# Kernel optimization log

Hardware: AMD Instinct MI355X
Metric: run time of the kernel (lower is better)

## Reference

```python
import jax, jax.numpy as jnp
import numpy as np

N_NODES = 100000
N_EDGES = 1600000
EMB = 128
N_LAYER = 5
X_DIM = 178
E_DIM = 18
BN_EPS = 1e-5


def setup_inputs() -> dict:
    key = jax.random.key(0)
    ks = jax.random.split(key, 20)
    s = 0.05  # weight scale
    inp = {}
    inp["x"] = jax.random.normal(ks[0], (N_NODES, X_DIM), jnp.float32)
    inp["edge_attr"] = jax.random.uniform(ks[1], (N_EDGES, E_DIM), jnp.float32)
    # input MLP (178 -> emb -> emb, LeakyReLU 0.1)
    inp["iw1"] = jax.random.normal(ks[2], (X_DIM, EMB), jnp.float32) * s
    inp["ib1"] = jax.random.normal(ks[3], (EMB,), jnp.float32) * s
    inp["iw2"] = jax.random.normal(ks[4], (EMB, EMB), jnp.float32) * s
    inp["ib2"] = jax.random.normal(ks[5], (EMB,), jnp.float32) * s
    # per-layer edge embedding MLP (18 -> emb -> emb, LeakyReLU 0.1)
    inp["ew1"] = jax.random.normal(ks[6], (N_LAYER, E_DIM, EMB), jnp.float32) * s
    inp["eb1"] = jax.random.normal(ks[7], (N_LAYER, EMB), jnp.float32) * s
    inp["ew2"] = jax.random.normal(ks[8], (N_LAYER, EMB, EMB), jnp.float32) * s
    inp["eb2"] = jax.random.normal(ks[9], (N_LAYER, EMB), jnp.float32) * s
    # per-layer GIN update MLP (emb -> 2emb -> emb, ReLU)
    inp["mw1"] = jax.random.normal(ks[10], (N_LAYER, EMB, 2 * EMB), jnp.float32) * s
    inp["mb1"] = jax.random.normal(ks[11], (N_LAYER, 2 * EMB), jnp.float32) * s
    inp["mw2"] = jax.random.normal(ks[12], (N_LAYER, 2 * EMB, EMB), jnp.float32) * s
    inp["mb2"] = jax.random.normal(ks[13], (N_LAYER, EMB), jnp.float32) * s
    # per-layer BatchNorm affine params
    inp["gamma"] = jnp.ones((N_LAYER, EMB), jnp.float32)
    inp["beta"] = jnp.zeros((N_LAYER, EMB), jnp.float32)
    inp["edge_index"] = jax.random.randint(ks[14], (2, N_EDGES), 0, N_NODES)
    return inp


def _leaky(v):
    return jnp.where(v > 0, v, 0.1 * v)


def reference(x, edge_attr, iw1, ib1, iw2, ib2, ew1, eb1, ew2, eb2,
              mw1, mb1, mw2, mb2, gamma, beta, edge_index):
    src = edge_index[0]  # x_j gathered from source nodes (PyG source_to_target)
    dst = edge_index[1]
    n = x.shape[0]

    # input node MLP with LeakyReLU(0.1)
    h = _leaky(x @ iw1 + ib1) @ iw2 + ib2  # [N, EMB]

    for l in range(N_LAYER):
        # edge embeddings for real edges: [E, EMB]
        ee = _leaky(edge_attr @ ew1[l] + eb1[l]) @ ew2[l] + eb2[l]
        # self-loop edges have zero edge_attr -> constant embedding vector [EMB]
        self_e = _leaky(eb1[l]) @ ew2[l] + eb2[l]
        # message = x_j + edge_emb; aggregate (add) at destination, plus self-loop term
        msg = h[src] + ee
        aggr = jax.ops.segment_sum(msg, dst, num_segments=n) + h + self_e
        # GIN update MLP (ReLU)
        hh = jnp.maximum(aggr @ mw1[l] + mb1[l], 0.0) @ mw2[l] + mb2[l]
        # BatchNorm1d (training mode: batch stats, biased variance)
        mean = hh.mean(axis=0)
        var = hh.var(axis=0)
        hh = (hh - mean) / jnp.sqrt(var + BN_EPS) * gamma[l] + beta[l]
        if l < N_LAYER - 1:
            hh = jnp.maximum(hh, 0.0)  # ReLU on all but last layer; dropout p=0 is a no-op
        h = hh

    return h  # JK == 'last'
```

## Files before the change

### kernel.cpp

```cpp
#include <hip/hip_runtime.h>
#include <hip/hip_bf16.h>
#include <hip/hip_fp16.h>
#include <cstdint>
#include <cstddef>

#define NNODES 100000
#define NEDGES 1600000
#define EMBD 128
#define NLAYER 5
#define XDIM 178
#define EDIM 18
#define BNEPS 1e-5f

typedef __attribute__((ext_vector_type(8))) short short8;
typedef __attribute__((ext_vector_type(8))) unsigned short ushort8;
typedef __attribute__((ext_vector_type(4))) float f32x4;

static __device__ __forceinline__ float leakyf(float v){ return v > 0.f ? v : 0.1f*v; }
static __device__ __forceinline__ unsigned short f2b(float v){
  __hip_bfloat16 b = __float2bfloat16(v);
  return *reinterpret_cast<unsigned short*>(&b);
}
static __device__ __forceinline__ float b2f(unsigned short u){
  __hip_bfloat16 b = *reinterpret_cast<__hip_bfloat16*>(&u);
  return __bfloat162float(b);
}
static __device__ __forceinline__ unsigned short f2h(float v){
  __half h = __float2half(v);
  return *reinterpret_cast<unsigned short*>(&h);
}
static __device__ __forceinline__ float h2f(unsigned short u){
  __half h = *reinterpret_cast<__half*>(&u);
  return __half2float(h);
}

__global__ __launch_bounds__(256) void k_hist(const int* __restrict__ dst, int* __restrict__ cnt){
  int e = blockIdx.x*256 + threadIdx.x;
  if (e < NEDGES) atomicAdd(&cnt[dst[e]], 1);
}

__global__ __launch_bounds__(256) void k_scan1(const int* __restrict__ cnt, int* __restrict__ rowptr,
                                               int* __restrict__ bsum){
  __shared__ int s[256];
  int t = threadIdx.x, i = blockIdx.x*256 + t;
  int v = (i < NNODES) ? cnt[i] : 0;
  s[t] = v; __syncthreads();
  for (int off=1; off<256; off<<=1){
    int x = (t>=off) ? s[t-off] : 0; __syncthreads();
    s[t] += x; __syncthreads();
  }
  if (i < NNODES) rowptr[i+1] = s[t];
  if (t == 255) bsum[blockIdx.x] = s[t];
}

__global__ __launch_bounds__(512) void k_scan2(const int* __restrict__ bsum, int* __restrict__ boff, int nb){
  __shared__ int s[512];
  int t = threadIdx.x;
  int v = (t < nb) ? bsum[t] : 0;
  s[t] = v; __syncthreads();
  for (int off=1; off<512; off<<=1){
    int x = (t>=off) ? s[t-off] : 0; __syncthreads();
    s[t] += x; __syncthreads();
  }
  if (t < nb) boff[t] = s[t] - v;
}

__global__ __launch_bounds__(256) void k_scan3(int* __restrict__ rowptr, const int* __restrict__ boff){
  int i = blockIdx.x*256 + threadIdx.x;
  if (i < NNODES) rowptr[i+1] += boff[i>>8];
  if (i == 0) rowptr[0] = 0;
}

__global__ __launch_bounds__(256) void k_curcopy(const int* __restrict__ rowptr, int* __restrict__ cursor){
  int i = blockIdx.x*256 + threadIdx.x;
  if (i < NNODES) cursor[i] = rowptr[i];
}

__global__ __launch_bounds__(256) void k_fill_pos(const int* __restrict__ dst, int* __restrict__ cursor,
                                                  int* __restrict__ einv){
  int e = blockIdx.x*256 + threadIdx.x;
  if (e >= NEDGES) return;
  int pos = atomicAdd(&cursor[dst[e]], 1);
  einv[pos] = e;
}

__global__ __launch_bounds__(256) void k_fill_ea(const int* __restrict__ einv, const int* __restrict__ src,
                                                 const float* __restrict__ ea,
                                                 int* __restrict__ srcp, unsigned short* __restrict__ eap24){
  int pos = blockIdx.x*256 + threadIdx.x;
  if (pos >= NEDGES) return;
  int e = einv[pos];
  srcp[pos] = src[e];
  const float* a = ea + (size_t)e*EDIM;
  float v[18];
  #pragma unroll
  for (int k=0;k<9;++k){
    float2 t = *(const float2*)(a + 2*k);
    v[2*k] = t.x; v[2*k+1] = t.y;
  }
  ushort8 r0, r1, r2;
  #pragma unroll
  for (int k=0;k<8;++k) r0[k] = f2b(v[k]);
  #pragma unroll
  for (int k=0;k<8;++k) r1[k] = f2b(v[8+k]);
  #pragma unroll
  for (int k=0;k<8;++k) r2[k] = 0;
  r2[0] = f2b(v[16]); r2[1] = f2b(v[17]);
  r2[2] = 0x3F80;
  unsigned short* o = eap24 + (size_t)pos*24;
  *reinterpret_cast<ushort8*>(o)      = r0;
  *reinterpret_cast<ushort8*>(o + 8)  = r1;
  *reinterpret_cast<ushort8*>(o + 16) = r2;
}

__global__ __launch_bounds__(256) void k_fill(const int* __restrict__ src, const int* __restrict__ dst,
                                              const float* __restrict__ ea, int* __restrict__ cursor,
                                              int* __restrict__ perm, int* __restrict__ srcp,
                                              float* __restrict__ eap){
  int e = blockIdx.x*256 + threadIdx.x;
  if (e >= NEDGES) return;
  int pos = atomicAdd(&cursor[dst[e]], 1);
  perm[pos] = e;
  srcp[pos] = src[e];
  if (eap){
    const float* a = ea + (size_t)e*EDIM;
    float* o = eap + (size_t)pos*EDIM;
    #pragma unroll
    for (int k=0;k<EDIM;++k) o[k] = a[k];
  }
}

__global__ __launch_bounds__(128) void k_selfe(const float* __restrict__ eb1, const float* __restrict__ ew2,
                                               const float* __restrict__ eb2, float* __restrict__ selfe){
  int l = blockIdx.x, c = threadIdx.x;
  const float* b1 = eb1 + l*EMBD;
  const float* w2 = ew2 + (size_t)l*EMBD*EMBD;
  float acc = eb2[l*EMBD + c];
  for (int j=0;j<EMBD;++j) acc += leakyf(b1[j]) * w2[j*EMBD + c];
  selfe[l*EMBD + c] = acc;
}

__global__ __launch_bounds__(256) void k_wc(const float* __restrict__ ew2, const float* __restrict__ mw1,
                                            float* __restrict__ wc){
  int idx = blockIdx.x*256 + threadIdx.x;
  int l = idx >> 15, rem = idx & 32767;
  int i = rem >> 8, n = rem & 255;
  const float* e = ew2 + (size_t)l*EMBD*EMBD + i*EMBD;
  const float* m = mw1 + (size_t)l*EMBD*2*EMBD + n;
  float acc = 0.f;
  #pragma unroll 4
  for (int j=0;j<EMBD;++j) acc += e[j]*m[(size_t)j*2*EMBD];
  wc[idx] = acc;
}

__global__ __launch_bounds__(256) void k_pack(const float* __restrict__ s1, int rows1,
                                              const float* __restrict__ s2, int Kreal,
                                              int Kpad, int N, __hip_bfloat16* __restrict__ out){
  int idx = blockIdx.x*256 + threadIdx.x;
  if (idx >= Kpad*N) return;
  int k = idx / N, n = idx - k*N;
  float v = 0.f;
  if (k < rows1) v = s1[(size_t)k*N + n];
  else if (k < Kreal) v = s2[(size_t)(k-rows1)*N + n];
  unsigned short hi = f2b(v);
  unsigned short lo = f2b(v - b2f(hi));
  size_t o = (size_t)(k>>5)*N*32 + (size_t)n*32 + (k&31);
  unsigned short* po = (unsigned short*)out;
  po[o] = hi;
  po[(size_t)Kpad*N + o] = lo;
}

__global__ __launch_bounds__(256) void k_edge2(
    const unsigned short* __restrict__ hh, const int* __restrict__ rowptr,
    const int* __restrict__ srcp, const unsigned short* __restrict__ eap24,
    const float* __restrict__ ew1l, const float* __restrict__ eb1l,
    const float* __restrict__ eb2l, const float* __restrict__ selfel,
    float* __restrict__ S1, float* __restrict__ base, int GG)
{
  int tid = threadIdx.x;
  if ((int)blockIdx.x < GG){
    int li = tid & 31;
    int c4 = li*4;
    float4 sf4 = *(const float4*)(selfel + c4);
    float4 e24 = *(const float4*)(eb2l + c4);
    int slot = blockIdx.x*8 + (tid>>5);
    const int NS = GG*8;
    for (int node = slot; node < NNODES; node += NS){
      int rs = rowptr[node], re = rowptr[node+1];
      f32x4 b = (f32x4)0.f;
      for (int c0 = rs; c0 < re; c0 += 8){
        int cnt = re - c0;
        #pragma unroll
        for (int p=0;p<8;++p){
          int e = c0 + p; if (e > re-1) e = re-1;
          float m = (p < cnt) ? 1.f : 0.f;
          int sp = srcp[e];
          uint2 hv = *(const uint2*)(hh + (size_t)sp*EMBD + c4);
          b[0] = fmaf(m, h2f((unsigned short)(hv.x & 0xffffu)), b[0]);
          b[1] = fmaf(m, h2f((unsigned short)(hv.x >> 16)),     b[1]);
          b[2] = fmaf(m, h2f((unsigned short)(hv.y & 0xffffu)), b[2]);
          b[3] = fmaf(m, h2f((unsigned short)(hv.y >> 16)),     b[3]);
        }
      }
      float deg = (float)(re - rs);
      uint2 hn = *(const uint2*)(hh + (size_t)node*EMBD + c4);
      float4 o;
      o.x = b[0] + h2f((unsigned short)(hn.x & 0xffffu)) + sf4.x + deg*e24.x;
      o.y = b[1] + h2f((unsigned short)(hn.x >> 16))     + sf4.y + deg*e24.y;
      o.z = b[2] + h2f((unsigned short)(hn.y & 0xffffu)) + sf4.z + deg*e24.z;
      o.w = b[3] + h2f((unsigned short)(hn.y >> 16))     + sf4.w + deg*e24.w;
      *(float4*)(base + (size_t)node*EMBD + c4) = o;
    }
  } else {
    int lane = tid & 63;
    int lr = lane & 15, kb = lane >> 4;

    short8 bh[8];
    #pragma unroll
    for (int nf=0; nf<8; ++nf){
      int col = nf*16 + lr;
      ushort8 hh8;
      #pragma unroll
      for (int j=0;j<8;++j){
        int k = kb*8 + j;
        float v = 0.f;
        if (k < EDIM) v = ew1l[k*EMBD + col];
        else if (k == EDIM) v = eb1l[col];
        hh8[j] = f2b(v);
      }
      bh[nf] = *reinterpret_cast<short8*>(&hh8);
    }

    auto loadC = [&](int c0, int re)->short8{
      int cnt = re - c0;
      int idx = c0 + lr; if (idx > re-1) idx = re-1;
      short8 af = (short8)0;
      if (kb < 3){
        ushort8 t = *reinterpret_cast<const ushort8*>(eap24 + (size_t)idx*24 + kb*8);
        af = *reinterpret_cast<short8*>(&t);
      }
      if (lr >= cnt) af = (short8)0;
      return af;
    };

    const int GS = gridDim.x - GG;
    int wid = (blockIdx.x - GG)*4 + (tid>>6);
    const int NW = GS*4;
    for (int nA = wid; nA < NNODES; nA += 2*NW){
      int nB = nA + NW;
      bool hasB = (nB < NNODES);
      int rsA = rowptr[nA], reA = rowptr[nA+1];
      int rsB = 0, reB = 0;
      if (hasB){ rsB = rowptr[nB]; reB = rowptr[nB+1]; }
      float sA[8], sB[8];
      #pragma unroll
      for (int nf=0;nf<8;++nf){ sA[nf]=0.f; sB[nf]=0.f; }
      int cA = rsA, cB = rsB;
      while (cA < reA || cB < reB){
        bool dA = cA < reA, dB = cB < reB;
        short8 afA = (short8)0, afB = (short8)0;
        if (dA) afA = loadC(cA, reA);
        if (dB) afB = loadC(cB, reB);
        if (dA){
          #pragma unroll
          for (int nf=0;nf<8;++nf){
            f32x4 acc = (f32x4)0.f;
            acc = __builtin_amdgcn_mfma_f32_16x16x32_bf16(afA, bh[nf], acc, 0,0,0);
            #pragma unroll
            for (int j=0;j<4;++j){
              float v = acc[j];
              sA[nf] = fmaf(0.55f, v, sA[nf]);
              sA[nf] = fmaf(0.45f, fabsf(v), sA[nf]);
            }
          }
        }
        if (dB){
          #pragma unroll
          for (int nf=0;nf<8;++nf){
            f32x4 acc = (f32x4)0.f;
            acc = __builtin_amdgcn_mfma_f32_16x16x32_bf16(afB, bh[nf], acc, 0,0,0);
            #pragma unroll
            for (int j=0;j<4;++j){
              float v = acc[j];
              sB[nf] = fmaf(0.55f, v, sB[nf]);
              sB[nf] = fmaf(0.45f, fabsf(v), sB[nf]);
            }
          }
        }
        cA += 16; cB += 16;
      }

      {
        #pragma unroll
        for (int nf=0;nf<8;++nf){
          float v = sA[nf];
          v += __shfl_xor(v, 16);
          v += __shfl_xor(v, 32);
          sA[nf] = v;
        }
        float va = sA[0], vb = sA[1];
        if (kb == 1){ va = sA[2]; vb = sA[3]; }
        if (kb == 2){ va = sA[4]; vb = sA[5]; }
        if (kb == 3){ va = sA[6]; vb = sA[7]; }
        S1[(size_t)nA*EMBD + kb*32 + lr]      = va;
        S1[(size_t)nA*EMBD + kb*32 + 16 + lr] = vb;
      }
      if (hasB){
        #pragma unroll
        for (int nf=0;nf<8;++nf){
          float v = sB[nf];
          v += __shfl_xor(v, 16);
          v += __shfl_xor(v, 32);
          sB[nf] = v;
        }
        float va = sB[0], vb = sB[1];
        if (kb == 1){ va = sB[2]; vb = sB[3]; }
        if (kb == 2){ va = sB[4]; vb = sB[5]; }
        if (kb == 3){ va = sB[6]; vb = sB[7]; }
        S1[(size_t)nB*EMBD + kb*32 + lr]      = va;
        S1[(size_t)nB*EMBD + kb*32 + 16 + lr] = vb;
      }
    }
  }
}

__global__ __launch_bounds__(256) void k_edge(
    const float* __restrict__ h, const int* __restrict__ rowptr,
    const int* __restrict__ perm, const int* __restrict__ srcp,
    const float* __restrict__ edge_attr, const float* __restrict__ eaperm,
    const float* __restrict__ ew1l, const float* __restrict__ eb1l,
    const float* __restrict__ eb2l, const float* __restrict__ selfel,
    float* __restrict__ S1, float* __restrict__ base)
{
  __shared__ float w1s[EDIM*EMBD];
  __shared__ float b1s[EMBD];
  int tid = threadIdx.x;
  for (int i = tid; i < EDIM*EMBD; i += 256) w1s[i] = ew1l[i];
  if (tid < EMBD) b1s[tid] = eb1l[tid];
  __syncthreads();
  int lane = tid & 63;
  int node = blockIdx.x*4 + (tid >> 6);
  if (node >= NNODES) return;
  int rs = rowptr[node], re = rowptr[node+1];
  int c0 = lane*2;
  float s1x=0.f, s1y=0.f, bx=0.f, by=0.f;
  for (int i = rs; i < re; ++i){
    int s = __builtin_amdgcn_readfirstlane(srcp[i]);
    const float* ea;
    if (eaperm){
      ea = eaperm + (size_t)__builtin_amdgcn_readfirstlane(i)*EDIM;
    } else {
      ea = edge_attr + (size_t)__builtin_amdgcn_readfirstlane(perm[i])*EDIM;
    }
    float2 hs = *(const float2*)(h + (size_t)s*EMBD + c0);
    bx += hs.x; by += hs.y;
    float d0 = b1s[c0], d1 = b1s[c0+1];
    #pragma unroll
    for (int k=0;k<EDIM;++k){
      float av = ea[k];
      d0 += av * w1s[k*EMBD + c0];
      d1 += av * w1s[k*EMBD + c0 + 1];
    }
    s1x += leakyf(d0); s1y += leakyf(d1);
  }
  float deg = (float)(re - rs);
  float2 hv = *(const float2*)(h + (size_t)node*EMBD + c0);
  *(float2*)(S1 + (size_t)node*EMBD + c0) = make_float2(s1x, s1y);
  float bvx = bx + hv.x + selfel[c0]   + deg*eb2l[c0];
  float bvy = by + hv.y + selfel[c0+1] + deg*eb2l[c0+1];
  *(float2*)(base + (size_t)node*EMBD + c0) = make_float2(bvx, bvy);
}

template<int BN, int WGM, int WGN, bool ALO, bool BLO, int ACT, bool STATS, bool OBF16, bool CONCAT, bool KCHK, bool ABF16>
__global__ __launch_bounds__(512) void k_mgemm(
    const float* __restrict__ Af, const float* __restrict__ A1,
    const __hip_bfloat16* __restrict__ Ab,
    int M, int Kreal, int Kpad, int lda,
    const __hip_bfloat16* __restrict__ Bp,
    const float* __restrict__ bias,
    float* __restrict__ Cf, __hip_bfloat16* __restrict__ Cb, int ldc,
    float* __restrict__ stats, unsigned short* __restrict__ Ch)
{
  static_assert(WGM*WGN == 8, "8 waves");
  constexpr int BM = 128;
  constexpr int MF = BM/(16*WGM);
  constexpr int NF = BN/(16*WGN);
  constexpr int LDS_ROW = 40;
  __shared__ __align__(16) unsigned short Ah[BM*LDS_ROW];
  __shared__ __align__(16) unsigned short Al[ALO ? BM*LDS_ROW : 8];
  __shared__ float ssum[STATS ? BN : 4];
  __shared__ float ssq [STATS ? BN : 4];

  int tid = threadIdx.x;
  int row0 = blockIdx.x*BM;
  int w = tid >> 6, lane = tid & 63;
  int wm = w / WGN, wn = w % WGN;
  int lr = lane & 15, kb = lane >> 4;
  int wrow = wm*MF*16, wcol = wn*NF*16;

  if (STATS && tid < BN){ ssum[tid] = 0.f; ssq[tid] = 0.f; }

  f32x4 acc[MF][NF];
  #pragma unroll
  for (int a=0;a<MF;++a)
    #pragma unroll
    for (int b=0;b<NF;++b) acc[a][b] = (f32x4)0.f;

  const size_t planeSz = (size_t)Kpad*BN;
  int sr = tid >> 2;
  int skq = (tid & 3)*8;
  int grow = row0 + sr;
  const int KS = Kpad >> 5;

  for (int ks = 0; ks < KS; ++ks){
    int k0 = ks << 5;
    int kg = k0 + skq;
    ushort8 hv, lv;
    if (ABF16){
      short8 raw = (short8)0;
      if (grow < M) raw = *reinterpret_cast<const short8*>((const unsigned short*)Ab + (size_t)grow*lda + kg);
      hv = *reinterpret_cast<ushort8*>(&raw);
    } else {
      float v[8];
      if (KCHK){
        #pragma unroll
        for (int i=0;i<8;++i)
          v[i] = (grow < M && kg+i < Kreal) ? Af[(size_t)grow*lda + kg + i] : 0.f;
      } else {
        const float* s;
        if (CONCAT) s = (kg < EMBD) ? (Af + (size_t)grow*lda + kg) : (A1 + (size_t)grow*lda + (kg - EMBD));
        else        s = Af + (size_t)grow*lda + kg;
        float4 p0 = make_float4(0,0,0,0), p1 = make_float4(0,0,0,0);
        if (grow < M){ p0 = *(const float4*)s; p1 = *(const float4*)(s+4); }
        v[0]=p0.x; v[1]=p0.y; v[2]=p0.z; v[3]=p0.w;
        v[4]=p1.x; v[5]=p1.y; v[6]=p1.z; v[7]=p1.w;
      }
      #pragma unroll
      for (int i=0;i<8;++i){
        unsigned short h16 = f2b(v[i]);
        hv[i] = h16;
        if (ALO) lv[i] = f2b(v[i] - b2f(h16));
      }
    }
    __syncthreads();
    *reinterpret_cast<ushort8*>(&Ah[sr*LDS_ROW + skq]) = hv;
    if (ALO && !ABF16) *reinterpret_cast<ushort8*>(&Al[sr*LDS_ROW + skq]) = lv;
    __syncthreads();

    short8 ah[MF], al[MF];
    #pragma unroll
    for (int mf=0; mf<MF; ++mf){
      int r = (wrow + mf*16 + lr)*LDS_ROW + kb*8;
      ah[mf] = *reinterpret_cast<const short8*>(&Ah[r]);
      if (ALO) al[mf] = *reinterpret_cast<const short8*>(&Al[r]);
    }
    const unsigned short* bb = (const unsigned short*)Bp + (size_t)ks*BN*32;
    short8 bh[NF], blv[NF];
    #pragma unroll
    for (int nf=0; nf<NF; ++nf){
      size_t off = (size_t)(wcol + nf*16 + lr)*32 + kb*8;
      bh[nf] = *reinterpret_cast<const short8*>(bb + off);
      if (BLO) blv[nf] = *reinterpret_cast<const short8*>(bb + planeSz + off);
    }
    #pragma unroll
    for (int mf=0; mf<MF; ++mf){
      #pragma unroll
      for (int nf=0; nf<NF; ++nf){
        acc[mf][nf] = __builtin_amdgcn_mfma_f32_16x16x32_bf16(ah[mf], bh[nf], acc[mf][nf], 0, 0, 0);
        if (BLO)
          acc[mf][nf] = __builtin_amdgcn_mfma_f32_16x16x32_bf16(ah[mf], blv[nf], acc[mf][nf], 0, 0, 0);
        if (ALO)
          acc[mf][nf] = __builtin_amdgcn_mfma_f32_16x16x32_bf16(al[mf], bh[nf], acc[mf][nf], 0, 0, 0);
      }
    }
  }

  float bcol[NF];
  #pragma unroll
  for (int nf=0; nf<NF; ++nf) bcol[nf] = bias ? bias[wcol + nf*16 + lr] : 0.f;
  float s[NF], sq[NF];
  #pragma unroll
  for (int nf=0; nf<NF; ++nf){ s[nf]=0.f; sq[nf]=0.f; }

  #pragma unroll
  for (int mf=0; mf<MF; ++mf){
    #pragma unroll
    for (int j=0; j<4; ++j){
      int r = row0 + wrow + mf*16 + kb*4 + j;
      if (r < M){
        #pragma unroll
        for (int nf=0; nf<NF; ++nf){
          int c = wcol + nf*16 + lr;
          float v = acc[mf][nf][j] + bcol[nf];
          if (ACT == 1) v = leakyf(v);
          if (ACT == 2) v = fmaxf(v, 0.f);
          if (OBF16) Cb[(size_t)r*ldc + c] = __float2bfloat16(v);
          else       Cf[(size_t)r*ldc + c] = v;
          if (Ch) Ch[(size_t)r*ldc + c] = f2h(v);
          if (STATS){ s[nf] += v; sq[nf] += v*v; }
        }
      }
    }
  }
  if (STATS){
    #pragma unroll
    for (int nf=0; nf<NF; ++nf){
      atomicAdd(&ssum[wcol + nf*16 + lr], s[nf]);
      atomicAdd(&ssq [wcol + nf*16 + lr], sq[nf]);
    }
    __syncthreads();
    if (tid < BN){
      atomicAdd(&stats[tid], ssum[tid]);
      atomicAdd(&stats[BN + tid], ssq[tid]);
    }
  }
}

__global__ __launch_bounds__(256) void k_bn(const float* __restrict__ hh, const float* __restrict__ stats,
                                            const float* __restrict__ gamma, const float* __restrict__ beta,
                                            float* __restrict__ out, unsigned short* __restrict__ outh,
                                            int dorelu){
  int idx = blockIdx.x*256 + threadIdx.x;
  if (idx >= NNODES*(EMBD/4)) return;
  int c0 = (idx & (EMBD/4 - 1)) * 4;
  float4 v = *(const float4*)(hh + (size_t)idx*4);
  float o[4] = {v.x, v.y, v.z, v.w};
  const float invN = 1.f / (float)NNODES;
  #pragma unroll
  for (int i=0;i<4;++i){
    int c = c0 + i;
    float mean = stats[c] * invN;
    float var  = stats[EMBD + c] * invN - mean*mean;
    float inv  = rsqrtf(fmaxf(var, 0.f) + BNEPS);
    float y = (o[i] - mean) * inv * gamma[c] + beta[c];
    if (dorelu) y = fmaxf(y, 0.f);
    o[i] = y;
  }
  if (out) *(float4*)(out + (size_t)idx*4) = make_float4(o[0],o[1],o[2],o[3]);
  if (outh){
    uint2 pk;
    pk.x = (unsigned)f2h(o[0]) | ((unsigned)f2h(o[1]) << 16);
    pk.y = (unsigned)f2h(o[2]) | ((unsigned)f2h(o[3]) << 16);
    *reinterpret_cast<uint2*>(outh + (size_t)idx*4) = pk;
  }
}

extern "C" void kernel_launch(void* const* d_in, const int* in_sizes, int n_in,
                              void* d_out, int out_size, void* d_ws, size_t ws_size,
                              hipStream_t stream)
{
  const float* x   = (const float*)d_in[0];
  const float* ea  = (const float*)d_in[1];
  const float* iw1 = (const float*)d_in[2];
  const float* ib1 = (const float*)d_in[3];
  const float* iw2 = (const float*)d_in[4];
  const float* ib2 = (const float*)d_in[5];
  const float* ew1 = (const float*)d_in[6];
  const float* eb1 = (const float*)d_in[7];
  const float* ew2 = (const float*)d_in[8];
  const float* eb2 = (const float*)d_in[9];
  const float* mw1 = (const float*)d_in[10];
  const float* mb1 = (const float*)d_in[11];
  const float* mw2 = (const float*)d_in[12];
  const float* mb2 = (const float*)d_in[13];
  const float* gamma = (const float*)d_in[14];
  const float* beta  = (const float*)d_in[15];
  const int* eidx = (const int*)d_in[16];
  const int* srcI = eidx;
  const int* dstI = eidx + NEDGES;

  char* p = (char*)d_ws;
  auto alloc = [&](size_t bytes)->char*{
    char* r = p; p += (bytes + 255) & ~(size_t)255; return r;
  };
  float* hbuf  = (float*)alloc((size_t)NNODES*EMBD*4);
  float* S1    = (float*)alloc((size_t)NNODES*EMBD*4);
  float* base  = (float*)alloc((size_t)NNODES*EMBD*4);
  __hip_bfloat16* tbuf = (__hip_bfloat16*)alloc((size_t)NNODES*2*EMBD*2);
  int* perm   = (int*)alloc((size_t)NEDGES*4);
  int* srcp   = (int*)alloc((size_t)NEDGES*4);
  int* rowptr = (int*)alloc((size_t)(NNODES+1)*4);
  int* cursor = (int*)alloc((size_t)NNODES*4);
  int* bsum   = (int*)alloc(4096);
  int* boff   = (int*)alloc(4096);
  float* selfe = (float*)alloc(NLAYER*EMBD*4);
  float* stats = (float*)alloc(2*EMBD*4);
  float* wc    = (float*)alloc((size_t)NLAYER*EMBD*2*EMBD*4);
  __hip_bfloat16* Bi1 = (__hip_bfloat16*)alloc((size_t)192*EMBD*2*2);
  __hip_bfloat16* Bi2 = (__hip_bfloat16*)alloc((size_t)EMBD*EMBD*2*2);
  __hip_bfloat16* B1  = (__hip_bfloat16*)alloc((size_t)NLAYER*256*256*2*2);
  __hip_bfloat16* B2  = (__hip_bfloat16*)alloc((size_t)NLAYER*256*EMBD*2*2);
  size_t used = (size_t)(p - (char*)d_ws);

  bool use_new = (ws_size >= used + (size_t)NEDGES*24*2 + (size_t)NNODES*EMBD*2 + 512);
  unsigned short* eap24 = nullptr;
  unsigned short* hh16 = nullptr;
  float* eaperm = nullptr;
  if (use_new){
    eap24 = (unsigned short*)alloc((size_t)NEDGES*24*2);
    hh16  = (unsigned short*)alloc((size_t)NNODES*EMBD*2);
  } else if (ws_size >= used + (size_t)NEDGES*EDIM*4 + 256){
    eaperm = (float*)alloc((size_t)NEDGES*EDIM*4);
  }

  hipMemsetAsync(cursor, 0, (size_t)NNODES*4, stream);
  k_hist<<<(NEDGES+255)/256, 256, 0, stream>>>(dstI, cursor);
  int nb = (NNODES+255)/256;
  k_scan1<<<nb, 256, 0, stream>>>(cursor, rowptr, bsum);
  k_scan2<<<1, 512, 0, stream>>>(bsum, boff, nb);
  k_scan3<<<(NNODES+255)/256, 256, 0, stream>>>(rowptr, boff);
  k_curcopy<<<(NNODES+255)/256, 256, 0, stream>>>(rowptr, cursor);
  if (use_new){
    k_fill_pos<<<(NEDGES+255)/256, 256, 0, stream>>>(dstI, cursor, perm);
    k_fill_ea<<<(NEDGES+255)/256, 256, 0, stream>>>(perm, srcI, ea, srcp, eap24);
  } else {
    k_fill<<<(NEDGES+255)/256, 256, 0, stream>>>(srcI, dstI, ea, cursor, perm, srcp, eaperm);
  }
  k_selfe<<<NLAYER, EMBD, 0, stream>>>(eb1, ew2, eb2, selfe);

  k_wc<<<(NLAYER*EMBD*2*EMBD)/256, 256, 0, stream>>>(ew2, mw1, wc);
  k_pack<<<(192*EMBD+255)/256, 256, 0, stream>>>(iw1, XDIM, iw1, XDIM, 192, EMBD, Bi1);
  k_pack<<<(EMBD*EMBD+255)/256, 256, 0, stream>>>(iw2, EMBD, iw2, EMBD, EMBD, EMBD, Bi2);
  for (int l=0; l<NLAYER; ++l){
    k_pack<<<(256*256+255)/256, 256, 0, stream>>>(
        wc + (size_t)l*EMBD*2*EMBD, EMBD, mw1 + (size_t)l*EMBD*2*EMBD, 256, 256, 256,
        B1 + (size_t)l*256*256*2);
    k_pack<<<(256*EMBD+255)/256, 256, 0, stream>>>(
        mw2 + (size_t)l*2*EMBD*EMBD, 256, mw2, 256, 256, EMBD,
        B2 + (size_t)l*256*EMBD*2);
  }

  const int gx = (NNODES + 127)/128;

  k_mgemm<128,4,2, true,true,1,false,false,false,true ,false><<<gx, 512, 0, stream>>>(
      x, nullptr, nullptr, NNODES, XDIM, 192, XDIM, Bi1, ib1, S1, nullptr, EMBD, nullptr, nullptr);
  k_mgemm<128,4,2, true,true,0,false,false,false,false,false><<<gx, 512, 0, stream>>>(
      S1, nullptr, nullptr, NNODES, EMBD, EMBD, EMBD, Bi2, ib2, hbuf, nullptr, EMBD, nullptr,
      use_new ? hh16 : nullptr);

  for (int l=0; l<NLAYER; ++l){
    hipMemsetAsync(stats, 0, 2*EMBD*4, stream);
    if (use_new){
      k_edge2<<<2048, 256, 0, stream>>>(
          hh16, rowptr, srcp, eap24,
          ew1 + (size_t)l*EDIM*EMBD, eb1 + l*EMBD, eb2 + l*EMBD, selfe + l*EMBD,
          S1, base, 1408);
    } else {
      k_edge<<<NNODES/4, 256, 0, stream>>>(
          hbuf, rowptr, perm, srcp, ea, eaperm,
          ew1 + (size_t)l*EDIM*EMBD, eb1 + l*EMBD, eb2 + l*EMBD, selfe + l*EMBD,
          S1, base);
    }
    k_mgemm<256,2,4, true,true,2,false,true ,true ,false,false><<<gx, 512, 0, stream>>>(
        S1, base, nullptr, NNODES, 256, 256, EMBD, B1 + (size_t)l*256*256*2,
        mb1 + l*2*EMBD, nullptr, tbuf, 2*EMBD, nullptr, nullptr);
    k_mgemm<128,4,2, false,false,0,true ,false,false,false,true ><<<gx, 512, 0, stream>>>(
        nullptr, nullptr, tbuf, NNODES, 256, 256, 2*EMBD, B2 + (size_t)l*256*EMBD*2,
        mb2 + l*EMBD, S1, nullptr, EMBD, stats, nullptr);
    float* outp; unsigned short* outh;
    if (l == NLAYER-1){ outp = (float*)d_out; outh = nullptr; }
    else if (use_new) { outp = nullptr;       outh = hh16;    }
    else              { outp = hbuf;          outh = nullptr; }
    k_bn<<<(NNODES*(EMBD/4)+255)/256, 256, 0, stream>>>(
        S1, stats, gamma + l*EMBD, beta + l*EMBD, outp, outh, (l < NLAYER-1) ? 1 : 0);
  }
}
```

Before: 1.888 ms.

## Precompute per-layer edge first-layer sums for all layers in one pass

Adds a kernel that reads each node's edge attributes once and computes the per-node summed edge-MLP hidden activations for all five layers, storing them in a large per-layer buffer. Each layer loop then runs only a plain neighbor-gather kernel for h and reads the precomputed S1 slice. This removes four of the five passes over edge attributes. In exchange it adds about 256MB of workspace writes and reads, and it only runs when the workspace is large enough.

```diff
diff --git a/kernel.cpp b/kernel.cpp
--- a/kernel.cpp
+++ b/kernel.cpp
@@ -168,6 +168,130 @@
   unsigned short* po = (unsigned short*)out;
   po[o] = hi;
   po[(size_t)Kpad*N + o] = lo;
+}
+
+__global__ __launch_bounds__(256) void k_s1all(
+    const int* __restrict__ rowptr, const unsigned short* __restrict__ eap24,
+    const float* __restrict__ ew1, const float* __restrict__ eb1,
+    float* __restrict__ S1all)
+{
+  __shared__ __align__(16) unsigned short wlds[NLAYER*3*EMBD*8];
+  int tid = threadIdx.x;
+  for (int i = tid; i < NLAYER*3*EMBD*8; i += 256){
+    int j = i & 7;
+    int col = (i >> 3) & 127;
+    int kb3 = (i >> 10) % 3;
+    int l = i / 3072;
+    int k = kb3*8 + j;
+    float v = 0.f;
+    if (k < EDIM) v = ew1[(size_t)l*EDIM*EMBD + k*EMBD + col];
+    else if (k == EDIM) v = eb1[l*EMBD + col];
+    wlds[i] = f2b(v);
+  }
+  __syncthreads();
+
+  int lane = tid & 63;
+  int lr = lane & 15, kb = lane >> 4;
+
+  int wid = blockIdx.x*4 + (tid>>6);
+  const int NW = gridDim.x*4;
+  for (int node = wid; node < NNODES; node += NW){
+    int rs = rowptr[node], re = rowptr[node+1];
+    float s[NLAYER][8];
+    #pragma unroll
+    for (int l=0;l<NLAYER;++l)
+      #pragma unroll
+      for (int nf=0;nf<8;++nf) s[l][nf] = 0.f;
+
+    for (int c0 = rs; c0 < re; c0 += 16){
+      int cnt = re - c0;
+      int idx = c0 + lr; if (idx > re-1) idx = re-1;
+      short8 af = (short8)0;
+      if (kb < 3){
+        ushort8 t = *reinterpret_cast<const ushort8*>(eap24 + (size_t)idx*24 + kb*8);
+        af = *reinterpret_cast<short8*>(&t);
+      }
+      if (lr >= cnt) af = (short8)0;
+
+      #pragma unroll
+      for (int l=0;l<NLAYER;++l){
+        #pragma unroll
+        for (int nf=0;nf<8;++nf){
+          short8 bh = (short8)0;
+          if (kb < 3)
+            bh = *reinterpret_cast<const short8*>(&wlds[(((l*3+kb)*128) + nf*16 + lr)*8]);
+          f32x4 acc = (f32x4)0.f;
+          acc = __builtin_amdgcn_mfma_f32_16x16x32_bf16(af, bh, acc, 0,0,0);
+          #pragma unroll
+          for (int j=0;j<4;++j){
+            float v = acc[j];
+            s[l][nf] = fmaf(0.55f, v, s[l][nf]);
+            s[l][nf] = fmaf(0.45f, fabsf(v), s[l][nf]);
+          }
+        }
+      }
+    }
+
+    #pragma unroll
+    for (int l=0;l<NLAYER;++l){
+      float r[8];
+      #pragma unroll
+      for (int nf=0;nf<8;++nf){
+        float v = s[l][nf];
+        v += __shfl_xor(v, 16);
+        v += __shfl_xor(v, 32);
+        r[nf] = v;
+      }
+      float va = r[0], vb = r[1];
+      if (kb == 1){ va = r[2]; vb = r[3]; }
+      if (kb == 2){ va = r[4]; vb = r[5]; }
+      if (kb == 3){ va = r[6]; vb = r[7]; }
+      float* dst = S1all + ((size_t)l*NNODES + node)*EMBD;
+      dst[kb*32 + lr]      = va;
+      dst[kb*32 + 16 + lr] = vb;
+    }
+  }
+}
+
+__global__ __launch_bounds__(256) void k_gather_h(
+    const unsigned short* __restrict__ hh,
+    const int* __restrict__ rowptr, const int* __restrict__ srcp,
+    const float* __restrict__ eb2l, const float* __restrict__ selfel,
+    float* __restrict__ base)
+{
+  int tid = threadIdx.x;
+  int li = tid & 31;
+  int c4 = li*4;
+  float4 sf4 = *(const float4*)(selfel + c4);
+  float4 e24 = *(const float4*)(eb2l + c4);
+  int slot = blockIdx.x*8 + (tid>>5);
+  const int NS = gridDim.x*8;
+  for (int node = slot; node < NNODES; node += NS){
+    int rs = rowptr[node], re = rowptr[node+1];
+    f32x4 b = (f32x4)0.f;
+    for (int c0 = rs; c0 < re; c0 += 8){
+      int cnt = re - c0;
+      #pragma unroll
+      for (int p=0;p<8;++p){
+        int e = c0 + p; if (e > re-1) e = re-1;
+        float m = (p < cnt) ? 1.f : 0.f;
+        int sp = srcp[e];
+        uint2 hv = *(const uint2*)(hh + (size_t)sp*EMBD + c4);
+        b[0] = fmaf(m, h2f((unsigned short)(hv.x & 0xffffu)), b[0]);
+        b[1] = fmaf(m, h2f((unsigned short)(hv.x >> 16)),     b[1]);
+        b[2] = fmaf(m, h2f((unsigned short)(hv.y & 0xffffu)), b[2]);
+        b[3] = fmaf(m, h2f((unsigned short)(hv.y >> 16)),     b[3]);
+      }
+    }
+    float deg = (float)(re - rs);
+    uint2 hn = *(const uint2*)(hh + (size_t)node*EMBD + c4);
+    float4 o;
+    o.x = b[0] + h2f((unsigned short)(hn.x & 0xffffu)) + sf4.x + deg*e24.x;
+    o.y = b[1] + h2f((unsigned short)(hn.x >> 16))     + sf4.y + deg*e24.y;
+    o.z = b[2] + h2f((unsigned short)(hn.y & 0xffffu)) + sf4.z + deg*e24.z;
+    o.w = b[3] + h2f((unsigned short)(hn.y >> 16))     + sf4.w + deg*e24.w;
+    *(float4*)(base + (size_t)node*EMBD + c4) = o;
+  }
 }
 
 __global__ __launch_bounds__(256) void k_edge2(
@@ -214,7 +338,6 @@
   } else {
     int lane = tid & 63;
     int lr = lane & 15, kb = lane >> 4;
-
     short8 bh[8];
     #pragma unroll
     for (int nf=0; nf<8; ++nf){
@@ -230,7 +353,6 @@
       }
       bh[nf] = *reinterpret_cast<short8*>(&hh8);
     }
-
     auto loadC = [&](int c0, int re)->short8{
       int cnt = re - c0;
       int idx = c0 + lr; if (idx > re-1) idx = re-1;
@@ -242,7 +364,6 @@
       if (lr >= cnt) af = (short8)0;
       return af;
     };
-
     const int GS = gridDim.x - GG;
     int wid = (blockIdx.x - GG)*4 + (tid>>6);
     const int NW = GS*4;
@@ -289,7 +410,6 @@
         }
         cA += 16; cB += 16;
       }
-
       {
         #pragma unroll
         for (int nf=0;nf<8;++nf){
@@ -592,16 +712,27 @@
   __hip_bfloat16* B2  = (__hip_bfloat16*)alloc((size_t)NLAYER*256*EMBD*2*2);
   size_t used = (size_t)(p - (char*)d_ws);
 
-  bool use_new = (ws_size >= used + (size_t)NEDGES*24*2 + (size_t)NNODES*EMBD*2 + 512);
+  const size_t szEap  = (size_t)NEDGES*24*2;
+  const size_t szHh   = (size_t)NNODES*EMBD*2;
+  const size_t szS1a  = (size_t)NLAYER*NNODES*EMBD*4;
+
+  bool tierA = (ws_size >= used + szEap + szHh + szS1a + 1024);
+  bool tierB = !tierA && (ws_size >= used + szEap + szHh + 512);
   unsigned short* eap24 = nullptr;
   unsigned short* hh16 = nullptr;
+  float* s1all = nullptr;
   float* eaperm = nullptr;
-  if (use_new){
-    eap24 = (unsigned short*)alloc((size_t)NEDGES*24*2);
-    hh16  = (unsigned short*)alloc((size_t)NNODES*EMBD*2);
+  if (tierA){
+    eap24 = (unsigned short*)alloc(szEap);
+    hh16  = (unsigned short*)alloc(szHh);
+    s1all = (float*)alloc(szS1a);
+  } else if (tierB){
+    eap24 = (unsigned short*)alloc(szEap);
+    hh16  = (unsigned short*)alloc(szHh);
   } else if (ws_size >= used + (size_t)NEDGES*EDIM*4 + 256){
     eaperm = (float*)alloc((size_t)NEDGES*EDIM*4);
   }
+  bool use_new = tierA || tierB;
 
   hipMemsetAsync(cursor, 0, (size_t)NNODES*4, stream);
   k_hist<<<(NEDGES+255)/256, 256, 0, stream>>>(dstI, cursor);
@@ -630,6 +761,9 @@
         B2 + (size_t)l*256*EMBD*2);
   }
 
+  if (tierA)
+    k_s1all<<<1024, 256, 0, stream>>>(rowptr, eap24, ew1, eb1, s1all);
+
   const int gx = (NNODES + 127)/128;
 
   k_mgemm<128,4,2, true,true,1,false,false,false,true ,false><<<gx, 512, 0, stream>>>(
@@ -640,7 +774,12 @@
 
   for (int l=0; l<NLAYER; ++l){
     hipMemsetAsync(stats, 0, 2*EMBD*4, stream);
-    if (use_new){
+    const float* s1p = S1;
+    if (tierA){
+      k_gather_h<<<2048, 256, 0, stream>>>(
+          hh16, rowptr, srcp, eb2 + l*EMBD, selfe + l*EMBD, base);
+      s1p = s1all + (size_t)l*NNODES*EMBD;
+    } else if (tierB){
       k_edge2<<<2048, 256, 0, stream>>>(
           hh16, rowptr, srcp, eap24,
           ew1 + (size_t)l*EDIM*EMBD, eb1 + l*EMBD, eb2 + l*EMBD, selfe + l*EMBD,
@@ -652,7 +791,7 @@
           S1, base);
     }
     k_mgemm<256,2,4, true,true,2,false,true ,true ,false,false><<<gx, 512, 0, stream>>>(
-        S1, base, nullptr, NNODES, 256, 256, EMBD, B1 + (size_t)l*256*256*2,
+        s1p, base, nullptr, NNODES, 256, 256, EMBD, B1 + (size_t)l*256*256*2,
         mb1 + l*2*EMBD, nullptr, tbuf, 2*EMBD, nullptr, nullptr);
     k_mgemm<128,4,2, false,false,0,true ,false,false,false,true ><<<gx, 512, 0, stream>>>(
         nullptr, nullptr, tbuf, NNODES, 256, 256, 2*EMBD, B2 + (size_t)l*256*EMBD*2,
```

Result: no change. 1.887 ms (-0.0%).
